# Performance work log

Measured on AMD Instinct MI355X. Metric: run time of the kernel, lower is better.

Reference implementation:

```python
import jax, jax.numpy as jnp
import numpy as np

N, E, G = 30000, 120000, 256
F_IN, F_E, H, T = 16, 8, 32, 10
EPS = 1e-5


def setup_inputs() -> dict:
    key = jax.random.key(0)
    ks = jax.random.split(key, 16)
    s = 0.05
    inp = {
        'x': jax.random.normal(ks[0], (N, F_IN), jnp.float32),
        'edge_attr': jax.random.normal(ks[1], (E, F_E), jnp.float32),
        'edge_index': jax.random.randint(ks[2], (2, E), 0, N),
        'batch': jnp.sort(jax.random.randint(ks[3], (N,), 0, G)),
        'c1_nn_w': jax.random.normal(ks[4], (F_E, F_IN * H), jnp.float32) * s,
        'c1_nn_b': jnp.zeros((F_IN * H,), jnp.float32),
        'c1_root': jax.random.normal(ks[5], (F_IN, H), jnp.float32) * s,
        'c1_bias': jnp.zeros((H,), jnp.float32),
        'c2_nn_w': jax.random.normal(ks[6], (F_E, H * H), jnp.float32) * s,
        'c2_nn_b': jnp.zeros((H * H,), jnp.float32),
        'c2_root': jax.random.normal(ks[7], (H, H), jnp.float32) * s,
        'c2_bias': jnp.zeros((H,), jnp.float32),
        'c3_nn_w': jax.random.normal(ks[8], (F_E, H * H), jnp.float32) * s,
        'c3_nn_b': jnp.zeros((H * H,), jnp.float32),
        'c3_root': jax.random.normal(ks[9], (H, H), jnp.float32) * s,
        'c3_bias': jnp.zeros((H,), jnp.float32),
        'bn1_g': jnp.ones((H,), jnp.float32), 'bn1_b': jnp.zeros((H,), jnp.float32),
        'bn1_m': jnp.zeros((H,), jnp.float32), 'bn1_v': jnp.ones((H,), jnp.float32),
        'bn2_g': jnp.ones((H,), jnp.float32), 'bn2_b': jnp.zeros((H,), jnp.float32),
        'bn2_m': jnp.zeros((H,), jnp.float32), 'bn2_v': jnp.ones((H,), jnp.float32),
        'mlp_w1': jax.random.normal(ks[10], (H, H), jnp.float32) * s,
        'mlp_b1': jnp.zeros((H,), jnp.float32),
        'mlp_w2': jax.random.normal(ks[11], (H, T), jnp.float32) * s,
        'mlp_b2': jnp.zeros((T,), jnp.float32),
    }
    return inp


def _nnconv(x, edge_index, edge_attr, nn_w, nn_b, root, bias, in_dim, out_dim):
    # per-edge weight matrix from edge features: [E, in_dim, out_dim]
    W = (edge_attr @ nn_w + nn_b).reshape(-1, in_dim, out_dim)
    # gather source node features, per-edge matvec, scatter-add to targets
    msg = jnp.einsum('ei,eio->eo', x[edge_index[0]], W)
    agg = jax.ops.segment_sum(msg, edge_index[1], num_segments=N)
    return agg + x @ root + bias


def _graph_size_norm(x, batch):
    deg = jax.ops.segment_sum(jnp.ones((N,), x.dtype), batch, num_segments=G)
    inv_sqrt = jnp.where(deg > 0, deg, 1.0) ** -0.5
    return x * inv_sqrt[batch][:, None]


def _bn_eval(x, g, b, m, v):
    return (x - m) * (g * jax.lax.rsqrt(v + EPS)) + b


def reference(x, edge_attr, edge_index, batch,
              c1_nn_w, c1_nn_b, c1_root, c1_bias,
              c2_nn_w, c2_nn_b, c2_root, c2_bias,
              c3_nn_w, c3_nn_b, c3_root, c3_bias,
              bn1_g, bn1_b, bn1_m, bn1_v,
              bn2_g, bn2_b, bn2_m, bn2_v,
              mlp_w1, mlp_b1, mlp_w2, mlp_b2):
    h = _nnconv(x, edge_index, edge_attr, c1_nn_w, c1_nn_b, c1_root, c1_bias, F_IN, H)
    h = _graph_size_norm(h, batch)
    h = jax.nn.relu(_bn_eval(h, bn1_g, bn1_b, bn1_m, bn1_v))
    h = _nnconv(h, edge_index, edge_attr, c2_nn_w, c2_nn_b, c2_root, c2_bias, H, H)
    h = _graph_size_norm(h, batch)
    h = jax.nn.relu(_bn_eval(h, bn2_g, bn2_b, bn2_m, bn2_v))
    h = _nnconv(h, edge_index, edge_attr, c3_nn_w, c3_nn_b, c3_root, c3_bias, H, H)
    # global mean pool over graphs
    cnt = jax.ops.segment_sum(jnp.ones((N,), h.dtype), batch, num_segments=G)
    pooled = jax.ops.segment_sum(h, batch, num_segments=G) / jnp.maximum(cnt, 1.0)[:, None]
    # MLP head (dropout inactive in eval)
    out = jax.nn.relu(pooled @ mlp_w1 + mlp_b1) @ mlp_w2 + mlp_b2
    return out
```

## Files before the change

kernel.cpp:

```cpp
#include <hip/hip_runtime.h>

#define NN 30000
#define NE 120000
#define NG 256
#define FIN 16
#define HD 32
#define TOUT 10
#define EPSV 1e-5f
#define CAP 32

__device__ __forceinline__ void atomAddF(float* p, float v) {
    unsafeAtomicAdd(p, v);
}

__global__ __launch_bounds__(256) void init_kernel(
    const int* __restrict__ batch,
    int*   __restrict__ cursor,
    float* __restrict__ deg_g,
    float* __restrict__ pooled)
{
    const int t = blockIdx.x * 256 + threadIdx.x;

    if (t < NN) cursor[t] = t * CAP;
    if (t < NG * HD) pooled[t] = 0.0f;

    if (t < NG) {
        int lo = 0, hi = NN;
        while (lo < hi) { const int m = (lo + hi) >> 1;
                          if (batch[m] < t) lo = m + 1; else hi = m; }
        const int b0 = lo;
        lo = 0; hi = NN;
        while (lo < hi) { const int m = (lo + hi) >> 1;
                          if (batch[m] < t + 1) lo = m + 1; else hi = m; }
        deg_g[t] = (float)(lo - b0);
    }
}

__global__ __launch_bounds__(256) void bucket_scatter(
    const int* __restrict__ eidx, const float* __restrict__ ea,
    int* __restrict__ cursor,
    int* __restrict__ src_b,
    float4* __restrict__ ea_b)
{
    const int e = blockIdx.x * 256 + threadIdx.x;
    if (e >= NE) return;
    const int d = eidx[NE + e];
    const int slot = atomicAdd(&cursor[d], 1);
    if (slot < d * CAP + CAP) {
        src_b[slot] = eidx[e];
        const float4* s4 = (const float4*)(ea + (size_t)e * 8);
        ea_b[2 * slot]     = s4[0];
        ea_b[2 * slot + 1] = s4[1];
    }
}

template<int IN, bool FINAL>
__global__ __launch_bounds__(256) void fused_layer(
    const float* __restrict__ hin,
    const int*   __restrict__ src_b,
    const float4* __restrict__ ea_b,
    const int*   __restrict__ cursor,
    const float* __restrict__ nn_w,
    const float* __restrict__ nn_b,
    const float* __restrict__ root,
    const float* __restrict__ bias,
    const int*   __restrict__ batch,
    const float* __restrict__ deg_g,
    const float* __restrict__ bn_g,
    const float* __restrict__ bn_b,
    const float* __restrict__ bn_m,
    const float* __restrict__ bn_v,
    float*       __restrict__ out)
{
    constexpr int K  = 10 * IN;
    constexpr int KQ = K / 4;
    constexpr int KL = KQ / 2;
    constexpr int NQ = 32 / IN;

    __shared__ float Tlds[16 * K];
    __shared__ float P[4 * 16 * 64];

    const int tid = threadIdx.x;
    const int wv  = tid >> 6;
    const int l   = tid & 63;
    const int h   = l >> 5;
    const int o   = l & 31;
    const int l5  = l & 31;
    const int pr  = l >> 5;

    float Wreg[KL];
    const int kbase = wv * KQ + h * KL;
    #pragma unroll
    for (int kk = 0; kk < KL; ++kk) {
        const int k = kbase + kk;
        const float* src = (k < 8 * IN) ? (nn_w + k * 32)
                         : (k < 9 * IN) ? (nn_b + (k - 8 * IN) * 32)
                                        : (root + (k - 9 * IN) * 32);
        Wreg[kk] = src[o];
    }

    const int i = l5 & (IN - 1);
    const int q = l5 / IN;

    #pragma unroll
    for (int j = 0; j < 2; ++j) {
        const int nloc = wv * 4 + j * 2 + pr;
        const int d    = blockIdx.x * 16 + nloc;

        float t[9];
        #pragma unroll
        for (int f = 0; f < 9; ++f) t[f] = 0.0f;

        const int p0 = d * CAP;
        int p1 = cursor[d];
        p1 = (p1 < p0 + CAP) ? p1 : (p0 + CAP);

        int p = p0 + q;
        if (p < p1) {
            const int pe = p1 - 1;
            int pn     = p + NQ;
            int pnc    = (pn < pe) ? pn : pe;
            int s_cur  = src_b[p];
            int s_nxt  = src_b[pnc];
            float4 a_c = ea_b[2 * p];
            float4 b_c = ea_b[2 * p + 1];
            float  xv  = hin[(long)s_cur * IN + i];

            while (true) {
                const float4 a_n = ea_b[2 * pnc];
                const float4 b_n = ea_b[2 * pnc + 1];
                const float  xvn = hin[(long)s_nxt * IN + i];
                const int pn2    = pn + NQ;
                const int pn2c   = (pn2 < pe) ? pn2 : pe;
                const int s_n2   = src_b[pn2c];

                t[0] = fmaf(a_c.x, xv, t[0]);
                t[1] = fmaf(a_c.y, xv, t[1]);
                t[2] = fmaf(a_c.z, xv, t[2]);
                t[3] = fmaf(a_c.w, xv, t[3]);
                t[4] = fmaf(b_c.x, xv, t[4]);
                t[5] = fmaf(b_c.y, xv, t[5]);
                t[6] = fmaf(b_c.z, xv, t[6]);
                t[7] = fmaf(b_c.w, xv, t[7]);
                t[8] += xv;

                p = pn;
                if (p >= p1) break;
                pn = pn2; pnc = pn2c; s_nxt = s_n2;
                a_c = a_n; b_c = b_n; xv = xvn;
            }
        }

        if (IN == 16) {
            #pragma unroll
            for (int f = 0; f < 9; ++f) t[f] += __shfl_xor(t[f], 16, 64);
        }

        if (l5 < IN) {
            float* tb = Tlds + nloc * K;
            #pragma unroll
            for (int f = 0; f < 9; ++f) tb[f * IN + i] = t[f];
            tb[9 * IN + i] = hin[(long)d * IN + i];
        }
    }
    __syncthreads();

    for (int n = 0; n < 16; ++n) {
        const float* tb = Tlds + n * K + kbase;
        float acc = 0.0f;
        #pragma unroll
        for (int kq = 0; kq < KL / 4; ++kq) {
            const float4 tv = *(const float4*)(tb + kq * 4);
            acc = fmaf(Wreg[4 * kq + 0], tv.x, acc);
            acc = fmaf(Wreg[4 * kq + 1], tv.y, acc);
            acc = fmaf(Wreg[4 * kq + 2], tv.z, acc);
            acc = fmaf(Wreg[4 * kq + 3], tv.w, acc);
        }
        P[(wv * 16 + n) * 64 + l] = acc;
    }
    __syncthreads();

    #pragma unroll
    for (int r = 0; r < 2; ++r) {
        const int idx = r * 256 + tid;
        const int n   = idx >> 5;
        const int oo  = idx & 31;
        float sum = bias[oo];
        #pragma unroll
        for (int ww = 0; ww < 4; ++ww) {
            const float* pb = P + (ww * 16 + n) * 64;
            sum += pb[oo] + pb[32 + oo];
        }
        const int d = blockIdx.x * 16 + n;
        const int g = batch[d];
        if (!FINAL) {
            float dg = deg_g[g];
            dg = dg > 0.0f ? dg : 1.0f;
            float v = sum * (1.0f / sqrtf(dg));
            const float s = bn_g[oo] / sqrtf(bn_v[oo] + EPSV);
            v = (v - bn_m[oo]) * s + bn_b[oo];
            out[(long)d * 32 + oo] = v > 0.0f ? v : 0.0f;
        } else {
            float v = sum;
            const int   g2 = __shfl(g, (tid & 63) ^ 32, 64);
            const float v2 = __shfl(v, (tid & 63) ^ 32, 64);
            bool do_store = true;
            if (g2 == g) {
                if (tid & 32) do_store = false;
                else          v += v2;
            }
            if (do_store) atomAddF(&out[g * 32 + oo], v);
        }
    }
}

__global__ __launch_bounds__(64) void head_kernel(
    const float* __restrict__ pooled,
    const float* __restrict__ deg,
    const float* __restrict__ w1,
    const float* __restrict__ b1,
    const float* __restrict__ w2,
    const float* __restrict__ b2,
    float*       __restrict__ out)
{
    const int g = blockIdx.x * 64 + threadIdx.x;
    if (g >= NG) return;
    float cnt = deg[g];
    cnt = cnt > 1.0f ? cnt : 1.0f;

    float p[HD];
    #pragma unroll
    for (int i = 0; i < HD; ++i) p[i] = pooled[g * HD + i] / cnt;

    float hid[HD];
    #pragma unroll
    for (int j = 0; j < HD; ++j) {
        float a = b1[j];
        #pragma unroll
        for (int i = 0; i < HD; ++i)
            a = fmaf(p[i], w1[i * HD + j], a);
        hid[j] = a > 0.0f ? a : 0.0f;
    }
    #pragma unroll
    for (int t = 0; t < TOUT; ++t) {
        float a = b2[t];
        #pragma unroll
        for (int j = 0; j < HD; ++j)
            a = fmaf(hid[j], w2[j * TOUT + t], a);
        out[g * TOUT + t] = a;
    }
}

extern "C" void kernel_launch(void* const* d_in, const int* in_sizes, int n_in,
                              void* d_out, int out_size, void* d_ws, size_t ws_size,
                              hipStream_t stream)
{
    const float* x        = (const float*)d_in[0];
    const float* ea       = (const float*)d_in[1];
    const int*   eidx     = (const int*)  d_in[2];
    const int*   batch    = (const int*)  d_in[3];
    const float* c1_nn_w  = (const float*)d_in[4];
    const float* c1_nn_b  = (const float*)d_in[5];
    const float* c1_root  = (const float*)d_in[6];
    const float* c1_bias  = (const float*)d_in[7];
    const float* c2_nn_w  = (const float*)d_in[8];
    const float* c2_nn_b  = (const float*)d_in[9];
    const float* c2_root  = (const float*)d_in[10];
    const float* c2_bias  = (const float*)d_in[11];
    const float* c3_nn_w  = (const float*)d_in[12];
    const float* c3_nn_b  = (const float*)d_in[13];
    const float* c3_root  = (const float*)d_in[14];
    const float* c3_bias  = (const float*)d_in[15];
    const float* bn1_g    = (const float*)d_in[16];
    const float* bn1_b    = (const float*)d_in[17];
    const float* bn1_m    = (const float*)d_in[18];
    const float* bn1_v    = (const float*)d_in[19];
    const float* bn2_g    = (const float*)d_in[20];
    const float* bn2_b    = (const float*)d_in[21];
    const float* bn2_m    = (const float*)d_in[22];
    const float* bn2_v    = (const float*)d_in[23];
    const float* mlp_w1   = (const float*)d_in[24];
    const float* mlp_b1   = (const float*)d_in[25];
    const float* mlp_w2   = (const float*)d_in[26];
    const float* mlp_b2   = (const float*)d_in[27];
    float* out = (float*)d_out;

    float*  h1     = (float*)d_ws;
    float*  h2     = h1 + NN * HD;
    float4* ea_b   = (float4*)(h2 + NN * HD);
    int*    src_b  = (int*)(ea_b + 2 * NN * CAP);
    int*    cursor = src_b + NN * CAP;
    float*  deg_g  = (float*)(cursor + NN);
    float*  pooled = deg_g + NG;

    const int egrid = (NE + 255) / 256;

    init_kernel<<<(NN + 255) / 256, 256, 0, stream>>>(batch, cursor, deg_g, pooled);

    bucket_scatter<<<egrid, 256, 0, stream>>>(eidx, ea, cursor, src_b, ea_b);

    const int lgrid = NN / 16;

    fused_layer<FIN, false><<<lgrid, 256, 0, stream>>>(
        x, src_b, ea_b, cursor, c1_nn_w, c1_nn_b, c1_root, c1_bias,
        batch, deg_g, bn1_g, bn1_b, bn1_m, bn1_v, h1);

    fused_layer<HD, false><<<lgrid, 256, 0, stream>>>(
        h1, src_b, ea_b, cursor, c2_nn_w, c2_nn_b, c2_root, c2_bias,
        batch, deg_g, bn2_g, bn2_b, bn2_m, bn2_v, h2);

    fused_layer<HD, true><<<lgrid, 256, 0, stream>>>(
        h2, src_b, ea_b, cursor, c3_nn_w, c3_nn_b, c3_root, c3_bias,
        batch, deg_g, nullptr, nullptr, nullptr, nullptr, pooled);

    head_kernel<<<(NG + 63) / 64, 64, 0, stream>>>(pooled, deg_g, mlp_w1, mlp_b1,
                                                   mlp_w2, mlp_b2, out);
}
```

Before: 236.4 us.

## Split fused NNConv layer into separate gather and GEMM kernels

```diff
diff --git a/kernel.cpp b/kernel.cpp
--- a/kernel.cpp
+++ b/kernel.cpp
@@ -54,12 +54,85 @@
     }
 }
 
-template<int IN, bool FINAL>
-__global__ __launch_bounds__(256) void fused_layer(
+template<int IN>
+__global__ __launch_bounds__(256) void gather_T(
     const float* __restrict__ hin,
     const int*   __restrict__ src_b,
     const float4* __restrict__ ea_b,
     const int*   __restrict__ cursor,
+    float*       __restrict__ T)
+{
+    constexpr int K  = 10 * IN;
+    constexpr int NQ = 32 / IN;
+
+    const int tid = threadIdx.x;
+    const int hw  = tid >> 5;
+    const int l5  = tid & 31;
+    const int d   = blockIdx.x * 8 + hw;
+
+    const int i = l5 & (IN - 1);
+    const int q = l5 / IN;
+
+    float t[9];
+    #pragma unroll
+    for (int f = 0; f < 9; ++f) t[f] = 0.0f;
+
+    const int p0 = d * CAP;
+    int p1 = cursor[d];
+    p1 = (p1 < p0 + CAP) ? p1 : (p0 + CAP);
+
+    int p = p0 + q;
+    if (p < p1) {
+        const int pe = p1 - 1;
+        int pn     = p + NQ;
+        int pnc    = (pn < pe) ? pn : pe;
+        int s_cur  = src_b[p];
+        int s_nxt  = src_b[pnc];
+        float4 a_c = ea_b[2 * p];
+        float4 b_c = ea_b[2 * p + 1];
+        float  xv  = hin[(long)s_cur * IN + i];
+
+        while (true) {
+            const float4 a_n = ea_b[2 * pnc];
+            const float4 b_n = ea_b[2 * pnc + 1];
+            const float  xvn = hin[(long)s_nxt * IN + i];
+            const int pn2    = pn + NQ;
+            const int pn2c   = (pn2 < pe) ? pn2 : pe;
+            const int s_n2   = src_b[pn2c];
+
+            t[0] = fmaf(a_c.x, xv, t[0]);
+            t[1] = fmaf(a_c.y, xv, t[1]);
+            t[2] = fmaf(a_c.z, xv, t[2]);
+            t[3] = fmaf(a_c.w, xv, t[3]);
+            t[4] = fmaf(b_c.x, xv, t[4]);
+            t[5] = fmaf(b_c.y, xv, t[5]);
+            t[6] = fmaf(b_c.z, xv, t[6]);
+            t[7] = fmaf(b_c.w, xv, t[7]);
+            t[8] += xv;
+
+            p = pn;
+            if (p >= p1) break;
+            pn = pn2; pnc = pn2c; s_nxt = s_n2;
+            a_c = a_n; b_c = b_n; xv = xvn;
+        }
+    }
+
+    if (IN == 16) {
+        #pragma unroll
+        for (int f = 0; f < 9; ++f) t[f] += __shfl_xor(t[f], 16, 64);
+    }
+
+    if (l5 < IN) {
+        float* tb = T + (long)d * K;
+        #pragma unroll
+        for (int f = 0; f < 9; ++f) tb[f * IN + i] = t[f];
+        tb[9 * IN + i] = hin[(long)d * IN + i];
+    }
+}
+
+template<int IN, bool FINAL>
+__global__ __launch_bounds__(256) void gemm_out(
+    const float* __restrict__ T,
     const float* __restrict__ nn_w,
     const float* __restrict__ nn_b,
     const float* __restrict__ root,
@@ -75,9 +148,7 @@
     constexpr int K  = 10 * IN;
     constexpr int KQ = K / 4;
     constexpr int KL = KQ / 2;
-    constexpr int NQ = 32 / IN;
-
-    __shared__ float Tlds[16 * K];
+
     __shared__ float P[4 * 16 * 64];
 
     const int tid = threadIdx.x;
@@ -85,8 +156,6 @@
     const int l   = tid & 63;
     const int h   = l >> 5;
     const int o   = l & 31;
-    const int l5  = l & 31;
-    const int pr  = l >> 5;
 
     float Wreg[KL];
     const int kbase = wv * KQ + h * KL;
@@ -99,74 +168,8 @@
         Wreg[kk] = src[o];
     }
 
-    const int i = l5 & (IN - 1);
-    const int q = l5 / IN;
-
-    #pragma unroll
-    for (int j = 0; j < 2; ++j) {
-        const int nloc = wv * 4 + j * 2 + pr;
-        const int d    = blockIdx.x * 16 + nloc;
-
-        float t[9];
-        #pragma unroll
-        for (int f = 0; f < 9; ++f) t[f] = 0.0f;
-
-        const int p0 = d * CAP;
-        int p1 = cursor[d];
-        p1 = (p1 < p0 + CAP) ? p1 : (p0 + CAP);
-
-        int p = p0 + q;
-        if (p < p1) {
-            const int pe = p1 - 1;
-            int pn     = p + NQ;
-            int pnc    = (pn < pe) ? pn : pe;
-            int s_cur  = src_b[p];
-            int s_nxt  = src_b[pnc];
-            float4 a_c = ea_b[2 * p];
-            float4 b_c = ea_b[2 * p + 1];
-            float  xv  = hin[(long)s_cur * IN + i];
-
-            while (true) {
-                const float4 a_n = ea_b[2 * pnc];
-                const float4 b_n = ea_b[2 * pnc + 1];
-                const float  xvn = hin[(long)s_nxt * IN + i];
-                const int pn2    = pn + NQ;
-                const int pn2c   = (pn2 < pe) ? pn2 : pe;
-                const int s_n2   = src_b[pn2c];
-
-                t[0] = fmaf(a_c.x, xv, t[0]);
-                t[1] = fmaf(a_c.y, xv, t[1]);
-                t[2] = fmaf(a_c.z, xv, t[2]);
-                t[3] = fmaf(a_c.w, xv, t[3]);
-                t[4] = fmaf(b_c.x, xv, t[4]);
-                t[5] = fmaf(b_c.y, xv, t[5]);
-                t[6] = fmaf(b_c.z, xv, t[6]);
-                t[7] = fmaf(b_c.w, xv, t[7]);
-                t[8] += xv;
-
-                p = pn;
-                if (p >= p1) break;
-                pn = pn2; pnc = pn2c; s_nxt = s_n2;
-                a_c = a_n; b_c = b_n; xv = xvn;
-            }
-        }
-
-        if (IN == 16) {
-            #pragma unroll
-            for (int f = 0; f < 9; ++f) t[f] += __shfl_xor(t[f], 16, 64);
-        }
-
-        if (l5 < IN) {
-            float* tb = Tlds + nloc * K;
-            #pragma unroll
-            for (int f = 0; f < 9; ++f) tb[f * IN + i] = t[f];
-            tb[9 * IN + i] = hin[(long)d * IN + i];
-        }
-    }
-    __syncthreads();
-
     for (int n = 0; n < 16; ++n) {
-        const float* tb = Tlds + n * K + kbase;
+        const float* tb = T + (long)(blockIdx.x * 16 + n) * K + kbase;
         float acc = 0.0f;
         #pragma unroll
         for (int kq = 0; kq < KL / 4; ++kq) {
@@ -292,6 +295,7 @@
     int*    cursor = src_b + NN * CAP;
     float*  deg_g  = (float*)(cursor + NN);
     float*  pooled = deg_g + NG;
+    float*  T      = pooled + NG * HD;
 
     const int egrid = (NE + 255) / 256;
 
@@ -299,18 +303,22 @@
 
     bucket_scatter<<<egrid, 256, 0, stream>>>(eidx, ea, cursor, src_b, ea_b);
 
-    const int lgrid = NN / 16;
-
-    fused_layer<FIN, false><<<lgrid, 256, 0, stream>>>(
-        x, src_b, ea_b, cursor, c1_nn_w, c1_nn_b, c1_root, c1_bias,
+    const int agrid = NN / 8;
+    const int bgrid = NN / 16;
+
+    gather_T<FIN><<<agrid, 256, 0, stream>>>(x, src_b, ea_b, cursor, T);
+    gemm_out<FIN, false><<<bgrid, 256, 0, stream>>>(
+        T, c1_nn_w, c1_nn_b, c1_root, c1_bias,
         batch, deg_g, bn1_g, bn1_b, bn1_m, bn1_v, h1);
 
-    fused_layer<HD, false><<<lgrid, 256, 0, stream>>>(
-        h1, src_b, ea_b, cursor, c2_nn_w, c2_nn_b, c2_root, c2_bias,
+    gather_T<HD><<<agrid, 256, 0, stream>>>(h1, src_b, ea_b, cursor, T);
+    gemm_out<HD, false><<<bgrid, 256, 0, stream>>>(
+        T, c2_nn_w, c2_nn_b, c2_root, c2_bias,
         batch, deg_g, bn2_g, bn2_b, bn2_m, bn2_v, h2);
 
-    fused_layer<HD, true><<<lgrid, 256, 0, stream>>>(
-        h2, src_b, ea_b, cursor, c3_nn_w, c3_nn_b, c3_root, c3_bias,
+    gather_T<HD><<<agrid, 256, 0, stream>>>(h2, src_b, ea_b, cursor, T);
+    gemm_out<HD, true><<<bgrid, 256, 0, stream>>>(
+        T, c3_nn_w, c3_nn_b, c3_root, c3_bias,
         batch, deg_g, nullptr, nullptr, nullptr, nullptr, pooled);
 
     head_kernel<<<(NG + 63) / 64, 64, 0, stream>>>(pooled, deg_g, mlp_w1, mlp_b1,
```

After: 310.6 us. +31.4%, slower.
